# Optimization experiments

Measured on AMD Instinct MI355X. Metric: run time of the kernel, lower is better.

Reference implementation:

```python
import jax, jax.numpy as jnp
import numpy as np

B, D, E, K, H = 16384, 4096, 64, 8, 128


def setup_inputs() -> dict:
    key = jax.random.key(0)
    ks = jax.random.split(key, 6)
    return {
        "r_pooled": jax.random.normal(ks[0], (B, D), jnp.float32),
        "step_frac": jnp.asarray(0.37, jnp.float32),
        "hidden_norm": jax.random.uniform(ks[1], (B,), jnp.float32),
        "confidence": jax.random.uniform(ks[2], (B,), jnp.float32),
        # params stored (in, out); equivalent math to torch Linear
        "W1": jax.random.normal(ks[3], (D + 3, H), jnp.float32) / np.sqrt(D + 3),
        "b1": jnp.zeros((H,), jnp.float32),
        "W2": jax.random.normal(ks[4], (H, E), jnp.float32) / np.sqrt(H),
        "b2": jnp.zeros((E,), jnp.float32),
    }


def reference(r_pooled, step_frac, hidden_norm, confidence, W1, b1, W2, b2):
    b = r_pooled.shape[0]
    step_col = step_frac * jnp.ones((b, 1), r_pooled.dtype)  # torch.full((B,1), step_frac)
    features = jnp.concatenate(
        [r_pooled, step_col, hidden_norm[:, None], confidence[:, None]], axis=-1
    )  # (B, D+3)
    h = jax.nn.silu(features @ W1 + b1)          # (B, 128)
    logits = h @ W2 + b2                         # (B, E)
    topk_vals, topk_idx = jax.lax.top_k(logits, K)
    topk_weights = jax.nn.softmax(topk_vals, axis=-1)
    weights = jnp.zeros_like(logits).at[jnp.arange(b)[:, None], topk_idx].set(topk_weights)
    return weights, logits
```

## Files before the change

kernel.cpp:

```cpp
#include <hip/hip_runtime.h>
#include <math.h>

#define DGL 4096
#define HGL 128
#define EGL 64
#define BM  32
#define NKC 128
#define DELTA 5e-4f

typedef short  short8 __attribute__((ext_vector_type(8)));
typedef float  f32x4  __attribute__((ext_vector_type(4)));

__device__ inline unsigned short bf16_rne(float x) {
    unsigned u = __float_as_uint(x);
    u += 0x7FFFu + ((u >> 16) & 1u);
    return (unsigned short)(u >> 16);
}

__device__ inline void split2(float x, short& hi, short& lo) {
    unsigned u = __float_as_uint(x);
    hi = (short)(u >> 16);
    float hif = __uint_as_float(u & 0xFFFF0000u);
    lo = (short)bf16_rne(x - hif);
}

__device__ inline void async_lds16(const void* g, void* lds) {
    __builtin_amdgcn_global_load_lds(
        (__attribute__((address_space(1))) void*)g,
        (__attribute__((address_space(3))) void*)lds, 16, 0, 0);
}

__global__ void pack_w1(const float* __restrict__ W1, unsigned short* __restrict__ wsB) {
    const int b   = blockIdx.x;
    const int kci = b >> 3, nt = b & 7;
    const int l   = threadIdx.x;
    const int quad = l >> 4, l15 = l & 15;
    short hi[8], lo[8];
#pragma unroll
    for (int j = 0; j < 8; ++j) {
        const int k = kci * 32 + quad * 8 + j;
        const float x = W1[(size_t)k * HGL + nt * 16 + l15];
        split2(x, hi[j], lo[j]);
    }
    short8 vh, vl;
#pragma unroll
    for (int j = 0; j < 8; ++j) { vh[j] = hi[j]; vl[j] = lo[j]; }
    *(short8*)(wsB + (size_t)kci * 8192 + ((nt * 2 + 0) * 64 + l) * 8) = vh;
    *(short8*)(wsB + (size_t)kci * 8192 + ((nt * 2 + 1) * 64 + l) * 8) = vl;
}

#define SMEM_BYTES (8192 + 32768 + 18432)

__global__ __launch_bounds__(256, 2) void router_main(
    const float* __restrict__ r_pooled, const float* __restrict__ step_frac,
    const float* __restrict__ hn, const float* __restrict__ cf,
    const float* __restrict__ W1, const float* __restrict__ b1,
    const float* __restrict__ W2, const float* __restrict__ b2,
    const unsigned short* __restrict__ wsB, int* __restrict__ flags,
    float* __restrict__ out_w, float* __restrict__ out_l)
{
    __shared__ __align__(16) char smem[SMEM_BYTES];
    char*  AsBase = smem;
    float* w2s = (float*)(smem + 8192);
    float* hs  = (float*)(smem + 8192 + 32768);
    float* ls  = (float*)smem;
    float* wt  = (float*)(smem + 8320);

    const int t = threadIdx.x;
    const int w = t >> 6, l = t & 63;
    const int quad = l >> 4, l15 = l & 15;
    const int row0 = blockIdx.x * BM;
    const int mt = w >> 1, nh = w & 1;

    for (int q = 0; q < 8; ++q) {
        const int sidx = (w * 8 + q) * 64 + l;
        async_lds16(W2 + sidx * 4, (char*)w2s + (w * 8 + q) * 1024);
    }

    const int arow = t >> 3, ablk = t & 7;
    const float* aSrc = r_pooled + (size_t)(row0 + arow) * DGL + ((ablk ^ (arow & 7)) << 2);

    auto issueA = [&](int kci, int buf) {
        async_lds16(aSrc + kci * 32, AsBase + buf * 4096 + w * 1024);
    };
    auto loadB = [&](int kci, short8* bh, short8* bl) {
        const unsigned short* base = wsB + (size_t)kci * 8192;
#pragma unroll
        for (int i = 0; i < 4; ++i) {
            const int nt = nh * 4 + i;
            bh[i] = *(const short8*)(base + ((nt * 2 + 0) * 64 + l) * 8);
            bl[i] = *(const short8*)(base + ((nt * 2 + 1) * 64 + l) * 8);
        }
    };

    f32x4 acc[4];
#pragma unroll
    for (int i = 0; i < 4; ++i) acc[i] = (f32x4){0.f, 0.f, 0.f, 0.f};

    const int rl = mt * 16 + l15;
    const int s  = l15 & 7;

    auto compute = [&](int buf, const short8* bh, const short8* bl) {
        const char* Asb = AsBase + buf * 4096;
        const int plo = ((quad << 1)) ^ s;
        const int phi = ((quad << 1) | 1) ^ s;
        f32x4 va = *(const f32x4*)(Asb + rl * 128 + plo * 16);
        f32x4 vb = *(const f32x4*)(Asb + rl * 128 + phi * 16);
        float fa[8];
#pragma unroll
        for (int j = 0; j < 4; ++j) { fa[j] = va[j]; fa[j + 4] = vb[j]; }
        short8 ahi, alo;
#pragma unroll
        for (int j = 0; j < 8; ++j) { short h, lo2; split2(fa[j], h, lo2); ahi[j] = h; alo[j] = lo2; }
#pragma unroll
        for (int i = 0; i < 4; ++i) {
            acc[i] = __builtin_amdgcn_mfma_f32_16x16x32_bf16(ahi, bh[i], acc[i], 0, 0, 0);
            acc[i] = __builtin_amdgcn_mfma_f32_16x16x32_bf16(ahi, bl[i], acc[i], 0, 0, 0);
            acc[i] = __builtin_amdgcn_mfma_f32_16x16x32_bf16(alo, bh[i], acc[i], 0, 0, 0);
        }
    };

    short8 bh0[4], bl0[4], bh1[4], bl1[4];
    loadB(0, bh0, bl0);
    issueA(0, 0);

    for (int kci = 0; kci < NKC; kci += 2) {
        __syncthreads();
        if (kci + 1 < NKC) { issueA(kci + 1, 1); loadB(kci + 1, bh1, bl1); }
        compute(0, bh0, bl0);
        __syncthreads();
        if (kci + 2 < NKC) { issueA(kci + 2, 0); loadB(kci + 2, bh0, bl0); }
        compute(1, bh1, bl1);
    }

    {
        const float sf = step_frac[0];
        const int rbase = row0 + mt * 16 + quad * 4;
        float hnv[4], cfv[4];
#pragma unroll
        for (int r = 0; r < 4; ++r) { hnv[r] = hn[rbase + r]; cfv[r] = cf[rbase + r]; }
#pragma unroll
        for (int i = 0; i < 4; ++i) {
            const int c = nh * 64 + i * 16 + l15;
            const float w96 = W1[(size_t)4096 * HGL + c];
            const float w97 = W1[(size_t)4097 * HGL + c];
            const float w98 = W1[(size_t)4098 * HGL + c];
            const float bb  = b1[c];
#pragma unroll
            for (int r = 0; r < 4; ++r) {
                const float x = acc[i][r] + sf * w96 + hnv[r] * w97 + cfv[r] * w98 + bb;
                hs[c * 36 + (mt * 16 + quad * 4 + r)] = x / (1.0f + expf(-x));
            }
        }
    }
    __syncthreads();

    const int mg = t >> 4, ng = t & 15;
    const int m0 = mg * 2, cn0 = ng * 4;
    float acc2[2][4];
#pragma unroll
    for (int i = 0; i < 2; ++i)
#pragma unroll
        for (int j = 0; j < 4; ++j) acc2[i][j] = 0.0f;

#pragma unroll 8
    for (int k = 0; k < HGL; ++k) {
        const float2 a = *(const float2*)&hs[k * 36 + m0];
        const float4 wv = *(const float4*)&w2s[k * 64 + cn0];
        acc2[0][0] = fmaf(a.x, wv.x, acc2[0][0]);
        acc2[0][1] = fmaf(a.x, wv.y, acc2[0][1]);
        acc2[0][2] = fmaf(a.x, wv.z, acc2[0][2]);
        acc2[0][3] = fmaf(a.x, wv.w, acc2[0][3]);
        acc2[1][0] = fmaf(a.y, wv.x, acc2[1][0]);
        acc2[1][1] = fmaf(a.y, wv.y, acc2[1][1]);
        acc2[1][2] = fmaf(a.y, wv.z, acc2[1][2]);
        acc2[1][3] = fmaf(a.y, wv.w, acc2[1][3]);
    }
#pragma unroll
    for (int j = 0; j < 4; ++j) {
        const float bv = b2[cn0 + j];
        acc2[0][j] += bv; acc2[1][j] += bv;
    }
    __syncthreads();

#pragma unroll
    for (int i = 0; i < 2; ++i) {
        const int row = row0 + m0 + i;
        float4 lv; lv.x = acc2[i][0]; lv.y = acc2[i][1]; lv.z = acc2[i][2]; lv.w = acc2[i][3];
        *(float4*)&out_l[(size_t)row * EGL + cn0] = lv;
#pragma unroll
        for (int j = 0; j < 4; ++j) ls[(m0 + i) * 65 + cn0 + j] = acc2[i][j];
    }
    for (int idx = t; idx < 32 * 65; idx += 256) wt[idx] = 0.0f;
    __syncthreads();

    if (t < BM) {
        float vals[9]; int idxs[9];
#pragma unroll
        for (int i = 0; i < 9; ++i) { vals[i] = -INFINITY; idxs[i] = 0; }
        for (int e = 0; e < EGL; ++e) {
            const float v = ls[t * 65 + e];
            if (v > vals[8]) {
                int p = 8;
                while (p > 0 && v > vals[p - 1]) { vals[p] = vals[p - 1]; idxs[p] = idxs[p - 1]; --p; }
                vals[p] = v; idxs[p] = e;
            }
        }
        flags[row0 + t] = (vals[7] - vals[8] < DELTA) ? 1 : 0;
        const float mx = vals[0];
        float wgt[8], ssum = 0.0f;
#pragma unroll
        for (int i = 0; i < 8; ++i) { wgt[i] = expf(vals[i] - mx); ssum += wgt[i]; }
        const float inv = 1.0f / ssum;
#pragma unroll
        for (int i = 0; i < 8; ++i) wt[t * 65 + idxs[i]] = wgt[i] * inv;
    }
    __syncthreads();

    for (int idx = t; idx < BM * EGL; idx += 256) {
        const int m = idx >> 6, e = idx & 63;
        out_w[(size_t)(row0 + m) * EGL + e] = wt[m * 65 + e];
    }
}

__global__ __launch_bounds__(256, 2) void refine_rows(
    const float* __restrict__ r_pooled, const float* __restrict__ step_frac,
    const float* __restrict__ hn, const float* __restrict__ cf,
    const float* __restrict__ W1, const float* __restrict__ b1,
    const float* __restrict__ W2, const float* __restrict__ b2,
    const int* __restrict__ flags, float* __restrict__ out_w, float* __restrict__ out_l)
{
    __shared__ int rlist[32];
    __shared__ int rcount;
    __shared__ __align__(16) float als[4][1024];
    __shared__ float hred[4][128];
    __shared__ float lbuf[4][64];
    __shared__ float wbuf[4][64];

    const int t = threadIdx.x;
    const int row0 = blockIdx.x * 32;
    if (t == 0) rcount = 0;
    __syncthreads();
    if (t < 32 && flags[row0 + t]) { int p = atomicAdd(&rcount, 1); rlist[p] = row0 + t; }
    __syncthreads();
    const int n = rcount;
    if (n == 0) return;

    const int c = t & 127, half = t >> 7;
    for (int g = 0; g < n; g += 4) {
        const int R = min(4, n - g);
        float pr[4] = {0.f, 0.f, 0.f, 0.f};
        for (int kc2 = 0; kc2 < DGL; kc2 += 1024) {
            __syncthreads();
            for (int i = 0; i < R; ++i)
                *(float4*)&als[i][t * 4] =
                    *(const float4*)&r_pooled[(size_t)rlist[g + i] * DGL + kc2 + t * 4];
            __syncthreads();
            const float* wp = W1 + (size_t)(kc2 + half * 512) * HGL + c;
            const float* ap = &als[0][half * 512];
#pragma unroll 4
            for (int j = 0; j < 512; ++j) {
                const float wv = wp[(size_t)j * HGL];
#pragma unroll
                for (int i = 0; i < 4; ++i) pr[i] += als[i][half * 512 + j] * wv;
            }
            (void)ap;
        }
        __syncthreads();
        if (half == 0) { for (int i = 0; i < 4; ++i) hred[i][c] = pr[i]; }
        __syncthreads();
        if (half == 1) { for (int i = 0; i < 4; ++i) hred[i][c] += pr[i]; }
        __syncthreads();
        if (t < 128) {
            const float sf = step_frac[0];
            const float w96 = W1[(size_t)4096 * HGL + t];
            const float w97 = W1[(size_t)4097 * HGL + t];
            const float w98 = W1[(size_t)4098 * HGL + t];
            const float bb  = b1[t];
            for (int i = 0; i < R; ++i) {
                const int r = rlist[g + i];
                const float x = hred[i][t] + sf * w96 + hn[r] * w97 + cf[r] * w98 + bb;
                hred[i][t] = x / (1.0f + expf(-x));
            }
        }
        __syncthreads();
        if (t < 64) {
            for (int i = 0; i < R; ++i) {
                float acc = b2[t];
                for (int k = 0; k < HGL; ++k) acc += hred[i][k] * W2[k * EGL + t];
                lbuf[i][t] = acc; wbuf[i][t] = 0.0f;
                out_l[(size_t)rlist[g + i] * EGL + t] = acc;
            }
        }
        __syncthreads();
        if (t < R) {
            float vals[8]; int idxs[8];
#pragma unroll
            for (int i = 0; i < 8; ++i) { vals[i] = -INFINITY; idxs[i] = 0; }
            for (int e = 0; e < EGL; ++e) {
                const float v = lbuf[t][e];
                if (v > vals[7]) {
                    int p = 7;
                    while (p > 0 && v > vals[p - 1]) { vals[p] = vals[p - 1]; idxs[p] = idxs[p - 1]; --p; }
                    vals[p] = v; idxs[p] = e;
                }
            }
            const float mx = vals[0];
            float wgt[8], ssum = 0.0f;
#pragma unroll
            for (int i = 0; i < 8; ++i) { wgt[i] = expf(vals[i] - mx); ssum += wgt[i]; }
            const float inv = 1.0f / ssum;
#pragma unroll
            for (int i = 0; i < 8; ++i) wbuf[t][idxs[i]] = wgt[i] * inv;
        }
        __syncthreads();
        if (t < 64) {
            for (int i = 0; i < R; ++i) out_w[(size_t)rlist[g + i] * EGL + t] = wbuf[i][t];
        }
        __syncthreads();
    }
}

extern "C" void kernel_launch(void* const* d_in, const int* in_sizes, int n_in,
                              void* d_out, int out_size, void* d_ws, size_t ws_size,
                              hipStream_t stream) {
    const float* r_pooled    = (const float*)d_in[0];
    const float* step_frac   = (const float*)d_in[1];
    const float* hidden_norm = (const float*)d_in[2];
    const float* confidence  = (const float*)d_in[3];
    const float* W1          = (const float*)d_in[4];
    const float* b1          = (const float*)d_in[5];
    const float* W2          = (const float*)d_in[6];
    const float* b2          = (const float*)d_in[7];

    const int B = in_sizes[2];
    float* out_w = (float*)d_out;
    float* out_l = out_w + (size_t)B * EGL;

    unsigned short* wsB = (unsigned short*)d_ws;
    int* flags = (int*)((char*)d_ws + (2u << 20));

    hipLaunchKernelGGL(pack_w1, dim3(1024), dim3(64), 0, stream, W1, wsB);
    hipLaunchKernelGGL(router_main, dim3(B / BM), dim3(256), 0, stream,
                       r_pooled, step_frac, hidden_norm, confidence,
                       W1, b1, W2, b2, wsB, flags, out_w, out_l);
    hipLaunchKernelGGL(refine_rows, dim3(B / 32), dim3(256), 0, stream,
                       r_pooled, step_frac, hidden_norm, confidence,
                       W1, b1, W2, b2, flags, out_w, out_l);
}
```

Measured before the change: 649.5 us.

## Restructure router into single-wave blocks with MFMA second layer and compacted refine list

The main kernel now uses one 64-thread wave per 32-row block that loads A fragments straight from global memory into registers, prefetching one step ahead, with no LDS staging and no barriers in the K loop. Each wave computes all 128 hidden columns for two 16-row tiles. The second layer now runs on MFMA with split-bf16 W2 packed by a new kernel. Rows near a top-k tie are appended to a global list via an atomic counter, and a fixed 256-block refine kernel handles only those rows. This removes barriers and LDS traffic in the main loop and avoids launching a refine block per row group, at the cost of lower occupancy per block and more register pressure.

```diff
diff --git a/kernel.cpp b/kernel.cpp
--- a/kernel.cpp
+++ b/kernel.cpp
@@ -4,8 +4,6 @@
 #define DGL 4096
 #define HGL 128
 #define EGL 64
-#define BM  32
-#define NKC 128
 #define DELTA 5e-4f
 
 typedef short  short8 __attribute__((ext_vector_type(8)));
@@ -16,289 +14,282 @@
     u += 0x7FFFu + ((u >> 16) & 1u);
     return (unsigned short)(u >> 16);
 }
-
 __device__ inline void split2(float x, short& hi, short& lo) {
     unsigned u = __float_as_uint(x);
     hi = (short)(u >> 16);
     float hif = __uint_as_float(u & 0xFFFF0000u);
     lo = (short)bf16_rne(x - hif);
 }
-
-__device__ inline void async_lds16(const void* g, void* lds) {
-    __builtin_amdgcn_global_load_lds(
-        (__attribute__((address_space(1))) void*)g,
-        (__attribute__((address_space(3))) void*)lds, 16, 0, 0);
-}
-
-__global__ void pack_w1(const float* __restrict__ W1, unsigned short* __restrict__ wsB) {
-    const int b   = blockIdx.x;
+__device__ inline void split8(const float* f, short8& hi, short8& lo) {
+#pragma unroll
+    for (int j = 0; j < 8; ++j) { short h, l2; split2(f[j], h, l2); hi[j] = h; lo[j] = l2; }
+}
+
+__global__ void pack_w1(const float* __restrict__ W1, unsigned short* __restrict__ wsB1) {
+    const int b = blockIdx.x;
     const int kci = b >> 3, nt = b & 7;
-    const int l   = threadIdx.x;
-    const int quad = l >> 4, l15 = l & 15;
-    short hi[8], lo[8];
+    const int l = threadIdx.x, quad = l >> 4, l15 = l & 15;
+    short8 vh, vl;
 #pragma unroll
     for (int j = 0; j < 8; ++j) {
         const int k = kci * 32 + quad * 8 + j;
-        const float x = W1[(size_t)k * HGL + nt * 16 + l15];
-        split2(x, hi[j], lo[j]);
-    }
+        short h, lo; split2(W1[(size_t)k * HGL + nt * 16 + l15], h, lo);
+        vh[j] = h; vl[j] = lo;
+    }
+    *(short8*)(wsB1 + (size_t)kci * 8192 + ((nt * 2 + 0) * 64 + l) * 8) = vh;
+    *(short8*)(wsB1 + (size_t)kci * 8192 + ((nt * 2 + 1) * 64 + l) * 8) = vl;
+}
+
+__global__ void pack_w2(const float* __restrict__ W2, unsigned short* __restrict__ wsB2,
+                        int* __restrict__ gcount) {
+    if (blockIdx.x == 0 && threadIdx.x == 0) *gcount = 0;
+    const int b = blockIdx.x;
+    const int kc2 = b >> 2, nt = b & 3;
+    const int l = threadIdx.x, quad = l >> 4, l15 = l & 15;
     short8 vh, vl;
 #pragma unroll
-    for (int j = 0; j < 8; ++j) { vh[j] = hi[j]; vl[j] = lo[j]; }
-    *(short8*)(wsB + (size_t)kci * 8192 + ((nt * 2 + 0) * 64 + l) * 8) = vh;
-    *(short8*)(wsB + (size_t)kci * 8192 + ((nt * 2 + 1) * 64 + l) * 8) = vl;
-}
-
-#define SMEM_BYTES (8192 + 32768 + 18432)
-
-__global__ __launch_bounds__(256, 2) void router_main(
+    for (int j = 0; j < 8; ++j) {
+        const int k = kc2 * 32 + quad * 8 + j;
+        short h, lo; split2(W2[k * EGL + nt * 16 + l15], h, lo);
+        vh[j] = h; vl[j] = lo;
+    }
+    *(short8*)(wsB2 + ((kc2 * 4 + nt) * 2 + 0) * 512 + l * 8) = vh;
+    *(short8*)(wsB2 + ((kc2 * 4 + nt) * 2 + 1) * 512 + l * 8) = vl;
+}
+
+__global__ __launch_bounds__(64, 1) void router_main(
+    const float* __restrict__ r_pooled, const float* __restrict__ step_frac,
+    const float* __restrict__ hn, const float* __restrict__ cf,
+    const float* __restrict__ W1, const float* __restrict__ b1,
+    const float* __restrict__ b2v,
+    const unsigned short* __restrict__ wsB1, const unsigned short* __restrict__ wsB2,
+    int* __restrict__ gcount, int* __restrict__ glist,
+    float* __restrict__ out_w, float* __restrict__ out_l)
+{
+    __shared__ float hs[32 * 132];
+    __shared__ float ls[32 * 65];
+    __shared__ float wt[32 * 65];
+
+    const int l = threadIdx.x;
+    const int quad = l >> 4, l15 = l & 15;
+    const int row0 = blockIdx.x * 32;
+
+    const float* aB0 = r_pooled + (size_t)(row0 + l15) * DGL + quad * 8;
+    const float* aB1 = aB0 + (size_t)16 * DGL;
+
+    f32x4 acc[2][8];
+#pragma unroll
+    for (int m = 0; m < 2; ++m)
+#pragma unroll
+        for (int nt = 0; nt < 8; ++nt) acc[m][nt] = (f32x4){0.f, 0.f, 0.f, 0.f};
+
+    float4 a0[4];
+    a0[0] = *(const float4*)(aB0);
+    a0[1] = *(const float4*)(aB0 + 4);
+    a0[2] = *(const float4*)(aB1);
+    a0[3] = *(const float4*)(aB1 + 4);
+
+    for (int kci = 0; kci < 128; ++kci) {
+        const int kn = (kci + 1 < 128) ? (kci + 1) : 127;
+        float4 a1[4];
+        a1[0] = *(const float4*)(aB0 + kn * 32);
+        a1[1] = *(const float4*)(aB0 + kn * 32 + 4);
+        a1[2] = *(const float4*)(aB1 + kn * 32);
+        a1[3] = *(const float4*)(aB1 + kn * 32 + 4);
+
+        const unsigned short* bp = wsB1 + (size_t)kci * 8192 + l * 8;
+        short8 b[16];
+#pragma unroll
+        for (int nt = 0; nt < 8; ++nt) {
+            b[2 * nt]     = *(const short8*)(bp + (2 * nt) * 512);
+            b[2 * nt + 1] = *(const short8*)(bp + (2 * nt + 1) * 512);
+        }
+
+        short8 ahi[2], alo[2];
+#pragma unroll
+        for (int m = 0; m < 2; ++m) {
+            float fa[8];
+#pragma unroll
+            for (int j = 0; j < 4; ++j) { fa[j] = a0[2 * m][j]; fa[j + 4] = a0[2 * m + 1][j]; }
+            split8(fa, ahi[m], alo[m]);
+        }
+#pragma unroll
+        for (int m = 0; m < 2; ++m)
+#pragma unroll
+            for (int nt = 0; nt < 8; ++nt) {
+                acc[m][nt] = __builtin_amdgcn_mfma_f32_16x16x32_bf16(ahi[m], b[2 * nt],     acc[m][nt], 0, 0, 0);
+                acc[m][nt] = __builtin_amdgcn_mfma_f32_16x16x32_bf16(ahi[m], b[2 * nt + 1], acc[m][nt], 0, 0, 0);
+                acc[m][nt] = __builtin_amdgcn_mfma_f32_16x16x32_bf16(alo[m], b[2 * nt],     acc[m][nt], 0, 0, 0);
+            }
+#pragma unroll
+        for (int i = 0; i < 4; ++i) a0[i] = a1[i];
+    }
+
+    {
+        const float sf = step_frac[0];
+        float hnv[8], cfv[8];
+#pragma unroll
+        for (int m = 0; m < 2; ++m)
+#pragma unroll
+            for (int r = 0; r < 4; ++r) {
+                const int row = row0 + m * 16 + quad * 4 + r;
+                hnv[m * 4 + r] = hn[row];
+                cfv[m * 4 + r] = cf[row];
+            }
+#pragma unroll
+        for (int nt = 0; nt < 8; ++nt) {
+            const int c = nt * 16 + l15;
+            const float w96 = W1[(size_t)4096 * HGL + c];
+            const float w97 = W1[(size_t)4097 * HGL + c];
+            const float w98 = W1[(size_t)4098 * HGL + c];
+            const float bb  = b1[c];
+#pragma unroll
+            for (int m = 0; m < 2; ++m)
+#pragma unroll
+                for (int r = 0; r < 4; ++r) {
+                    const float x = acc[m][nt][r] + sf * w96 + hnv[m * 4 + r] * w97
+                                  + cfv[m * 4 + r] * w98 + bb;
+                    hs[(m * 16 + quad * 4 + r) * 132 + c] = x / (1.0f + expf(-x));
+                }
+        }
+    }
+    __syncthreads();
+
+    f32x4 acc2[2][4];
+#pragma unroll
+    for (int m = 0; m < 2; ++m)
+#pragma unroll
+        for (int nt = 0; nt < 4; ++nt) acc2[m][nt] = (f32x4){0.f, 0.f, 0.f, 0.f};
+
+#pragma unroll
+    for (int kc2 = 0; kc2 < 4; ++kc2) {
+        const unsigned short* bp2 = wsB2 + kc2 * 4096 + l * 8;
+        short8 c2[8];
+#pragma unroll
+        for (int nt = 0; nt < 4; ++nt) {
+            c2[2 * nt]     = *(const short8*)(bp2 + (2 * nt) * 512);
+            c2[2 * nt + 1] = *(const short8*)(bp2 + (2 * nt + 1) * 512);
+        }
+#pragma unroll
+        for (int m = 0; m < 2; ++m) {
+            const float4 va = *(const float4*)&hs[(m * 16 + l15) * 132 + kc2 * 32 + quad * 8];
+            const float4 vb = *(const float4*)&hs[(m * 16 + l15) * 132 + kc2 * 32 + quad * 8 + 4];
+            float fa[8];
+#pragma unroll
+            for (int j = 0; j < 4; ++j) { fa[j] = ((const float*)&va)[j]; fa[j + 4] = ((const float*)&vb)[j]; }
+            short8 h2, lo2v;
+            split8(fa, h2, lo2v);
+#pragma unroll
+            for (int nt = 0; nt < 4; ++nt) {
+                acc2[m][nt] = __builtin_amdgcn_mfma_f32_16x16x32_bf16(h2,   c2[2 * nt],     acc2[m][nt], 0, 0, 0);
+                acc2[m][nt] = __builtin_amdgcn_mfma_f32_16x16x32_bf16(h2,   c2[2 * nt + 1], acc2[m][nt], 0, 0, 0);
+                acc2[m][nt] = __builtin_amdgcn_mfma_f32_16x16x32_bf16(lo2v, c2[2 * nt],     acc2[m][nt], 0, 0, 0);
+            }
+        }
+    }
+
+#pragma unroll
+    for (int m = 0; m < 2; ++m)
+#pragma unroll
+        for (int nt = 0; nt < 4; ++nt) {
+            const int c = nt * 16 + l15;
+            const float bv = b2v[c];
+#pragma unroll
+            for (int r = 0; r < 4; ++r) {
+                const int lr = m * 16 + quad * 4 + r;
+                const float v = acc2[m][nt][r] + bv;
+                out_l[(size_t)(row0 + lr) * EGL + c] = v;
+                ls[lr * 65 + c] = v;
+            }
+        }
+    for (int i = l; i < 32 * 65; i += 64) wt[i] = 0.0f;
+    __syncthreads();
+
+    if (l < 32) {
+        float vals[9]; int idxs[9];
+#pragma unroll
+        for (int i = 0; i < 9; ++i) { vals[i] = -INFINITY; idxs[i] = 0; }
+        for (int e = 0; e < EGL; ++e) {
+            const float v = ls[l * 65 + e];
+            if (v > vals[8]) {
+                int p = 8;
+                while (p > 0 && v > vals[p - 1]) { vals[p] = vals[p - 1]; idxs[p] = idxs[p - 1]; --p; }
+                vals[p] = v; idxs[p] = e;
+            }
+        }
+        const float mx = vals[0];
+        float wgt[8], ssum = 0.0f;
+#pragma unroll
+        for (int i = 0; i < 8; ++i) { wgt[i] = expf(vals[i] - mx); ssum += wgt[i]; }
+        const float inv = 1.0f / ssum;
+#pragma unroll
+        for (int i = 0; i < 8; ++i) wt[l * 65 + idxs[i]] = wgt[i] * inv;
+        if (vals[7] - vals[8] < DELTA) {
+            int p = atomicAdd(gcount, 1);
+            if (p < 16384) glist[p] = row0 + l;
+        }
+    }
+    __syncthreads();
+
+    for (int i = l; i < 32 * EGL; i += 64) {
+        const int m = i >> 6, c = i & 63;
+        out_w[(size_t)(row0 + m) * EGL + c] = wt[m * 65 + c];
+    }
+}
+
+__global__ __launch_bounds__(512, 1) void refine_rows(
     const float* __restrict__ r_pooled, const float* __restrict__ step_frac,
     const float* __restrict__ hn, const float* __restrict__ cf,
     const float* __restrict__ W1, const float* __restrict__ b1,
     const float* __restrict__ W2, const float* __restrict__ b2,
-    const unsigned short* __restrict__ wsB, int* __restrict__ flags,
-    float* __restrict__ out_w, float* __restrict__ out_l)
+    const int* __restrict__ gcount, const int* __restrict__ glist,
+    float* __restrict__ out_w)
 {
-    __shared__ __align__(16) char smem[SMEM_BYTES];
-    char*  AsBase = smem;
-    float* w2s = (float*)(smem + 8192);
-    float* hs  = (float*)(smem + 8192 + 32768);
-    float* ls  = (float*)smem;
-    float* wt  = (float*)(smem + 8320);
+    __shared__ __align__(16) float als[DGL];
+    __shared__ float part[4][128];
+    __shared__ float hred[128];
+    __shared__ float lb[64];
+    __shared__ float wb[64];
 
     const int t = threadIdx.x;
-    const int w = t >> 6, l = t & 63;
-    const int quad = l >> 4, l15 = l & 15;
-    const int row0 = blockIdx.x * BM;
-    const int mt = w >> 1, nh = w & 1;
-
-    for (int q = 0; q < 8; ++q) {
-        const int sidx = (w * 8 + q) * 64 + l;
-        async_lds16(W2 + sidx * 4, (char*)w2s + (w * 8 + q) * 1024);
-    }
-
-    const int arow = t >> 3, ablk = t & 7;
-    const float* aSrc = r_pooled + (size_t)(row0 + arow) * DGL + ((ablk ^ (arow & 7)) << 2);
-
-    auto issueA = [&](int kci, int buf) {
-        async_lds16(aSrc + kci * 32, AsBase + buf * 4096 + w * 1024);
-    };
-    auto loadB = [&](int kci, short8* bh, short8* bl) {
-        const unsigned short* base = wsB + (size_t)kci * 8192;
-#pragma unroll
-        for (int i = 0; i < 4; ++i) {
-            const int nt = nh * 4 + i;
-            bh[i] = *(const short8*)(base + ((nt * 2 + 0) * 64 + l) * 8);
-            bl[i] = *(const short8*)(base + ((nt * 2 + 1) * 64 + l) * 8);
-        }
-    };
-
-    f32x4 acc[4];
-#pragma unroll
-    for (int i = 0; i < 4; ++i) acc[i] = (f32x4){0.f, 0.f, 0.f, 0.f};
-
-    const int rl = mt * 16 + l15;
-    const int s  = l15 & 7;
-
-    auto compute = [&](int buf, const short8* bh, const short8* bl) {
-        const char* Asb = AsBase + buf * 4096;
-        const int plo = ((quad << 1)) ^ s;
-        const int phi = ((quad << 1) | 1) ^ s;
-        f32x4 va = *(const f32x4*)(Asb + rl * 128 + plo * 16);
-        f32x4 vb = *(const f32x4*)(Asb + rl * 128 + phi * 16);
-        float fa[8];
-#pragma unroll
-        for (int j = 0; j < 4; ++j) { fa[j] = va[j]; fa[j + 4] = vb[j]; }
-        short8 ahi, alo;
-#pragma unroll
-        for (int j = 0; j < 8; ++j) { short h, lo2; split2(fa[j], h, lo2); ahi[j] = h; alo[j] = lo2; }
-#pragma unroll
-        for (int i = 0; i < 4; ++i) {
-            acc[i] = __builtin_amdgcn_mfma_f32_16x16x32_bf16(ahi, bh[i], acc[i], 0, 0, 0);
-            acc[i] = __builtin_amdgcn_mfma_f32_16x16x32_bf16(ahi, bl[i], acc[i], 0, 0, 0);
-            acc[i] = __builtin_amdgcn_mfma_f32_16x16x32_bf16(alo, bh[i], acc[i], 0, 0, 0);
-        }
-    };
-
-    short8 bh0[4], bl0[4], bh1[4], bl1[4];
-    loadB(0, bh0, bl0);
-    issueA(0, 0);
-
-    for (int kci = 0; kci < NKC; kci += 2) {
-        __syncthreads();
-        if (kci + 1 < NKC) { issueA(kci + 1, 1); loadB(kci + 1, bh1, bl1); }
-        compute(0, bh0, bl0);
-        __syncthreads();
-        if (kci + 2 < NKC) { issueA(kci + 2, 0); loadB(kci + 2, bh0, bl0); }
-        compute(1, bh1, bl1);
-    }
-
-    {
-        const float sf = step_frac[0];
-        const int rbase = row0 + mt * 16 + quad * 4;
-        float hnv[4], cfv[4];
-#pragma unroll
-        for (int r = 0; r < 4; ++r) { hnv[r] = hn[rbase + r]; cfv[r] = cf[rbase + r]; }
-#pragma unroll
-        for (int i = 0; i < 4; ++i) {
-            const int c = nh * 64 + i * 16 + l15;
-            const float w96 = W1[(size_t)4096 * HGL + c];
-            const float w97 = W1[(size_t)4097 * HGL + c];
-            const float w98 = W1[(size_t)4098 * HGL + c];
-            const float bb  = b1[c];
-#pragma unroll
-            for (int r = 0; r < 4; ++r) {
-                const float x = acc[i][r] + sf * w96 + hnv[r] * w97 + cfv[r] * w98 + bb;
-                hs[c * 36 + (mt * 16 + quad * 4 + r)] = x / (1.0f + expf(-x));
-            }
-        }
-    }
-    __syncthreads();
-
-    const int mg = t >> 4, ng = t & 15;
-    const int m0 = mg * 2, cn0 = ng * 4;
-    float acc2[2][4];
-#pragma unroll
-    for (int i = 0; i < 2; ++i)
-#pragma unroll
-        for (int j = 0; j < 4; ++j) acc2[i][j] = 0.0f;
-
+    const int cnt = *gcount;
+    const int c = t & 127, sl = t >> 7;
+
+    for (int i = blockIdx.x; i < cnt; i += gridDim.x) {
+        const int row = glist[i];
+        __syncthreads();
+        for (int j = t; j < DGL / 4; j += 512)
+            *(float4*)&als[j * 4] = *(const float4*)&r_pooled[(size_t)row * DGL + j * 4];
+        __syncthreads();
+
+        float pr = 0.0f;
+        const float* ap = als + sl * 1024;
+        const float* wp = W1 + (size_t)(sl * 1024) * HGL + c;
 #pragma unroll 8
-    for (int k = 0; k < HGL; ++k) {
-        const float2 a = *(const float2*)&hs[k * 36 + m0];
-        const float4 wv = *(const float4*)&w2s[k * 64 + cn0];
-        acc2[0][0] = fmaf(a.x, wv.x, acc2[0][0]);
-        acc2[0][1] = fmaf(a.x, wv.y, acc2[0][1]);
-        acc2[0][2] = fmaf(a.x, wv.z, acc2[0][2]);
-        acc2[0][3] = fmaf(a.x, wv.w, acc2[0][3]);
-        acc2[1][0] = fmaf(a.y, wv.x, acc2[1][0]);
-        acc2[1][1] = fmaf(a.y, wv.y, acc2[1][1]);
-        acc2[1][2] = fmaf(a.y, wv.z, acc2[1][2]);
-        acc2[1][3] = fmaf(a.y, wv.w, acc2[1][3]);
-    }
-#pragma unroll
-    for (int j = 0; j < 4; ++j) {
-        const float bv = b2[cn0 + j];
-        acc2[0][j] += bv; acc2[1][j] += bv;
-    }
-    __syncthreads();
-
-#pragma unroll
-    for (int i = 0; i < 2; ++i) {
-        const int row = row0 + m0 + i;
-        float4 lv; lv.x = acc2[i][0]; lv.y = acc2[i][1]; lv.z = acc2[i][2]; lv.w = acc2[i][3];
-        *(float4*)&out_l[(size_t)row * EGL + cn0] = lv;
-#pragma unroll
-        for (int j = 0; j < 4; ++j) ls[(m0 + i) * 65 + cn0 + j] = acc2[i][j];
-    }
-    for (int idx = t; idx < 32 * 65; idx += 256) wt[idx] = 0.0f;
-    __syncthreads();
-
-    if (t < BM) {
-        float vals[9]; int idxs[9];
-#pragma unroll
-        for (int i = 0; i < 9; ++i) { vals[i] = -INFINITY; idxs[i] = 0; }
-        for (int e = 0; e < EGL; ++e) {
-            const float v = ls[t * 65 + e];
-            if (v > vals[8]) {
-                int p = 8;
-                while (p > 0 && v > vals[p - 1]) { vals[p] = vals[p - 1]; idxs[p] = idxs[p - 1]; --p; }
-                vals[p] = v; idxs[p] = e;
-            }
-        }
-        flags[row0 + t] = (vals[7] - vals[8] < DELTA) ? 1 : 0;
-        const float mx = vals[0];
-        float wgt[8], ssum = 0.0f;
-#pragma unroll
-        for (int i = 0; i < 8; ++i) { wgt[i] = expf(vals[i] - mx); ssum += wgt[i]; }
-        const float inv = 1.0f / ssum;
-#pragma unroll
-        for (int i = 0; i < 8; ++i) wt[t * 65 + idxs[i]] = wgt[i] * inv;
-    }
-    __syncthreads();
-
-    for (int idx = t; idx < BM * EGL; idx += 256) {
-        const int m = idx >> 6, e = idx & 63;
-        out_w[(size_t)(row0 + m) * EGL + e] = wt[m * 65 + e];
-    }
-}
-
-__global__ __launch_bounds__(256, 2) void refine_rows(
-    const float* __restrict__ r_pooled, const float* __restrict__ step_frac,
-    const float* __restrict__ hn, const float* __restrict__ cf,
-    const float* __restrict__ W1, const float* __restrict__ b1,
-    const float* __restrict__ W2, const float* __restrict__ b2,
-    const int* __restrict__ flags, float* __restrict__ out_w, float* __restrict__ out_l)
-{
-    __shared__ int rlist[32];
-    __shared__ int rcount;
-    __shared__ __align__(16) float als[4][1024];
-    __shared__ float hred[4][128];
-    __shared__ float lbuf[4][64];
-    __shared__ float wbuf[4][64];
-
-    const int t = threadIdx.x;
-    const int row0 = blockIdx.x * 32;
-    if (t == 0) rcount = 0;
-    __syncthreads();
-    if (t < 32 && flags[row0 + t]) { int p = atomicAdd(&rcount, 1); rlist[p] = row0 + t; }
-    __syncthreads();
-    const int n = rcount;
-    if (n == 0) return;
-
-    const int c = t & 127, half = t >> 7;
-    for (int g = 0; g < n; g += 4) {
-        const int R = min(4, n - g);
-        float pr[4] = {0.f, 0.f, 0.f, 0.f};
-        for (int kc2 = 0; kc2 < DGL; kc2 += 1024) {
-            __syncthreads();
-            for (int i = 0; i < R; ++i)
-                *(float4*)&als[i][t * 4] =
-                    *(const float4*)&r_pooled[(size_t)rlist[g + i] * DGL + kc2 + t * 4];
-            __syncthreads();
-            const float* wp = W1 + (size_t)(kc2 + half * 512) * HGL + c;
-            const float* ap = &als[0][half * 512];
-#pragma unroll 4
-            for (int j = 0; j < 512; ++j) {
-                const float wv = wp[(size_t)j * HGL];
-#pragma unroll
-                for (int i = 0; i < 4; ++i) pr[i] += als[i][half * 512 + j] * wv;
-            }
-            (void)ap;
-        }
-        __syncthreads();
-        if (half == 0) { for (int i = 0; i < 4; ++i) hred[i][c] = pr[i]; }
-        __syncthreads();
-        if (half == 1) { for (int i = 0; i < 4; ++i) hred[i][c] += pr[i]; }
-        __syncthreads();
+        for (int k = 0; k < 1024; ++k) pr = fmaf(ap[k], wp[(size_t)k * HGL], pr);
+        part[sl][c] = pr;
+        __syncthreads();
+
         if (t < 128) {
             const float sf = step_frac[0];
-            const float w96 = W1[(size_t)4096 * HGL + t];
-            const float w97 = W1[(size_t)4097 * HGL + t];
-            const float w98 = W1[(size_t)4098 * HGL + t];
-            const float bb  = b1[t];
-            for (int i = 0; i < R; ++i) {
-                const int r = rlist[g + i];
-                const float x = hred[i][t] + sf * w96 + hn[r] * w97 + cf[r] * w98 + bb;
-                hred[i][t] = x / (1.0f + expf(-x));
-            }
+            float x = part[0][t] + part[1][t] + part[2][t] + part[3][t];
+            x += sf * W1[(size_t)4096 * HGL + t] + hn[row] * W1[(size_t)4097 * HGL + t]
+               + cf[row] * W1[(size_t)4098 * HGL + t] + b1[t];
+            hred[t] = x / (1.0f + expf(-x));
         }
         __syncthreads();
         if (t < 64) {
-            for (int i = 0; i < R; ++i) {
-                float acc = b2[t];
-                for (int k = 0; k < HGL; ++k) acc += hred[i][k] * W2[k * EGL + t];
-                lbuf[i][t] = acc; wbuf[i][t] = 0.0f;
-                out_l[(size_t)rlist[g + i] * EGL + t] = acc;
-            }
-        }
-        __syncthreads();
-        if (t < R) {
+            float a = b2[t];
+            for (int k = 0; k < HGL; ++k) a = fmaf(hred[k], W2[k * EGL + t], a);
+            lb[t] = a; wb[t] = 0.0f;
+        }
+        __syncthreads();
+        if (t == 0) {
             float vals[8]; int idxs[8];
 #pragma unroll
-            for (int i = 0; i < 8; ++i) { vals[i] = -INFINITY; idxs[i] = 0; }
+            for (int q = 0; q < 8; ++q) { vals[q] = -INFINITY; idxs[q] = 0; }
             for (int e = 0; e < EGL; ++e) {
-                const float v = lbuf[t][e];
+                const float v = lb[e];
                 if (v > vals[7]) {
                     int p = 7;
                     while (p > 0 && v > vals[p - 1]) { vals[p] = vals[p - 1]; idxs[p] = idxs[p - 1]; --p; }
@@ -308,16 +299,13 @@
             const float mx = vals[0];
             float wgt[8], ssum = 0.0f;
 #pragma unroll
-            for (int i = 0; i < 8; ++i) { wgt[i] = expf(vals[i] - mx); ssum += wgt[i]; }
+            for (int q = 0; q < 8; ++q) { wgt[q] = expf(vals[q] - mx); ssum += wgt[q]; }
             const float inv = 1.0f / ssum;
 #pragma unroll
-            for (int i = 0; i < 8; ++i) wbuf[t][idxs[i]] = wgt[i] * inv;
-        }
-        __syncthreads();
-        if (t < 64) {
-            for (int i = 0; i < R; ++i) out_w[(size_t)rlist[g + i] * EGL + t] = wbuf[i][t];
-        }
-        __syncthreads();
+            for (int q = 0; q < 8; ++q) wb[idxs[q]] = wgt[q] * inv;
+        }
+        __syncthreads();
+        if (t < 64) out_w[(size_t)row * EGL + t] = wb[t];
     }
 }
 
@@ -337,14 +325,17 @@
     float* out_w = (float*)d_out;
     float* out_l = out_w + (size_t)B * EGL;
 
-    unsigned short* wsB = (unsigned short*)d_ws;
-    int* flags = (int*)((char*)d_ws + (2u << 20));
-
-    hipLaunchKernelGGL(pack_w1, dim3(1024), dim3(64), 0, stream, W1, wsB);
-    hipLaunchKernelGGL(router_main, dim3(B / BM), dim3(256), 0, stream,
+    unsigned short* wsB1 = (unsigned short*)d_ws;
+    unsigned short* wsB2 = (unsigned short*)((char*)d_ws + 2097152);
+    int* gcount = (int*)((char*)d_ws + 2129920);
+    int* glist  = (int*)((char*)d_ws + 2129984);
+
+    hipLaunchKernelGGL(pack_w1, dim3(1024), dim3(64), 0, stream, W1, wsB1);
+    hipLaunchKernelGGL(pack_w2, dim3(16), dim3(64), 0, stream, W2, wsB2, gcount);
+    hipLaunchKernelGGL(router_main, dim3(B / 32), dim3(64), 0, stream,
                        r_pooled, step_frac, hidden_norm, confidence,
-                       W1, b1, W2, b2, wsB, flags, out_w, out_l);
-    hipLaunchKernelGGL(refine_rows, dim3(B / 32), dim3(256), 0, stream,
+                       W1, b1, b2, wsB1, wsB2, gcount, glist, out_w, out_l);
+    hipLaunchKernelGGL(refine_rows, dim3(256), dim3(512), 0, stream,
                        r_pooled, step_frac, hidden_norm, confidence,
-                       W1, b1, W2, b2, flags, out_w, out_l);
-}
+                       W1, b1, W2, b2, gcount, glist, out_w);
+}
```

New measurement: 619.8 us. 4.6% less time.
